# Performance work log

Hardware: AMD Instinct MI355X
Metric: run time of the kernel (lower is better)

The kernel has to match this reference:

```python
import jax, jax.numpy as jnp
import numpy as np

B, N = 4096, 8192
PULSE_LO = 40.0 / 60.0   # Hz
PULSE_HI = 250.0 / 60.0  # Hz


def setup_inputs() -> dict:
    key = jax.random.key(0)
    k1, k2 = jax.random.split(key)
    outputs = jax.random.normal(k1, (B, N), dtype=jnp.float32)
    # reference heart rates in Hz, uniform inside the pulse band
    targets = jax.random.uniform(k2, (B, 1), dtype=jnp.float32,
                                 minval=PULSE_LO, maxval=PULSE_HI)
    return {"outputs": outputs, "targets": targets, "Fs": 20}


def reference(outputs, targets, Fs):
    n = outputs.shape[-1]
    F = n // 2 + 1
    f = jnp.linspace(0.0, Fs / 2.0, F, dtype=jnp.float32)  # [F]

    min_idx = jnp.argmin(jnp.abs(f - PULSE_LO))
    max_idx = jnp.argmin(jnp.abs(f - PULSE_HI))

    # normalized rFFT power spectrum (torch.rfft(..., normalized=True) divides by sqrt(N))
    X = jnp.fft.rfft(outputs) * (1.0 / np.sqrt(n))          # [B, F] complex
    P1 = X.real ** 2 + X.imag ** 2                          # [B, F]

    # per-sample reference bin index
    r = jnp.argmin(jnp.abs(f[None, :] - targets.reshape(-1, 1)), axis=1)  # [B]
    rb = r[:, None]                                         # [B, 1]
    i = jnp.arange(F)[None, :]                              # [1, F]

    # signal mask u: 1 at ref and 1st harmonic, 0.5 at ref+-1 (applied after, as in torch)
    u = jnp.where((i == rb - 1) | (i == rb + 1), 0.5,
                  jnp.where((i == rb) | (i == 2 * rb), 1.0, 0.0))
    # noise mask w = 1 - u, zeroed outside pulse band and around 1st harmonic
    w = jnp.where((i < min_idx) | (i >= max_idx) |
                  (i == 2 * rb - 1) | (i == 2 * rb + 1),
                  0.0, 1.0 - u)

    signal_energy = jnp.sum(P1 * u, axis=1)                 # [B]
    noise_energy = jnp.sum(P1 * w, axis=1)                  # [B]
    losses = -10.0 * jnp.log(signal_energy / (noise_energy + 1.0)) / jnp.log(10.0)
    return jnp.mean(losses)
```

## Files before the change

### kernel.cpp

```cpp
#include <hip/hip_runtime.h>
#include <math.h>

#define TPB 256

typedef float cplx __attribute__((ext_vector_type(2)));

__device__ __forceinline__ cplx cmul(cplx a, cplx b) {
    return a.xx * b + cplx{-a.y, a.y} * b.yx;
}

__device__ __forceinline__ int sw2(int i) { return i ^ ((i >> 4) & 15); }

__device__ __forceinline__ void dft4(cplx& a, cplx& b, cplx& c, cplx& d) {
    cplx t0 = a + c, t1 = a - c, t2 = b + d, t3 = b - d;
    a = t0 + t2;
    c = t0 - t2;
    cplx jt3 = cplx{t3.y, -t3.x};
    b = t1 + jt3;
    d = t1 - jt3;
}

__device__ __forceinline__ void dft16(cplx v[16]) {
#pragma unroll
    for (int j = 0; j < 4; ++j) dft4(v[j], v[4 + j], v[8 + j], v[12 + j]);
    const float C1 = 0.9238795325112867f, S1 = 0.3826834323650898f;
    const float R2 = 0.7071067811865476f;
    v[5]  = cmul(v[5],  cplx{ C1, -S1});
    v[9]  = cmul(v[9],  cplx{ R2, -R2});
    v[13] = cmul(v[13], cplx{ S1, -C1});
    v[6]  = cmul(v[6],  cplx{ R2, -R2});
    v[10] = cplx{v[10].y, -v[10].x};
    v[14] = cmul(v[14], cplx{-R2, -R2});
    v[7]  = cmul(v[7],  cplx{ S1, -C1});
    v[11] = cmul(v[11], cplx{-R2, -R2});
    v[15] = cmul(v[15], cplx{-C1,  S1});
#pragma unroll
    for (int b = 0; b < 4; ++b) dft4(v[4 * b], v[4 * b + 1], v[4 * b + 2], v[4 * b + 3]);
}

__global__ __launch_bounds__(TPB, 4) void snr_kernel(const float* __restrict__ x,
                                                     const float* __restrict__ targets,
                                                     float* __restrict__ out) {
    __shared__ __align__(16) cplx Z[4096];
    float* zf = (float*)Z;

    const int t = threadIdx.x;
    const int blk = blockIdx.x;

    int r;
    {
        float tg = targets[blk];
        const float df = 0.00244140625f;
        int c0 = (int)(tg * 409.6f) - 2;
        if (c0 < 0) c0 = 0;
        r = c0;
        float best = fabsf(df * (float)c0 - tg);
        for (int i = c0 + 1; i <= c0 + 4 && i <= 4096; ++i) {
            float dd = fabsf(df * (float)i - tg);
            if (dd < best) { best = dd; r = i; }
        }
    }

    cplx v[16];
    const cplx* row = (const cplx*)(x + (size_t)blk * 8192);
#pragma unroll
    for (int l = 0; l < 16; ++l) v[l] = row[t + 256 * l];

    dft16(v);
    {
        float ang = -1.5339807878856412e-3f * (float)t;
        float sn, cs; __sincosf(ang, &sn, &cs);
        cplx w1 = cplx{cs, sn};
        cplx w2 = cmul(w1, w1), w3 = cmul(w2, w1);
        cplx w4 = cmul(w2, w2), w8 = cmul(w4, w4), w12 = cmul(w8, w4);
        cplx wa[4] = {cplx{1.f, 0.f}, w1, w2, w3};
        cplx wb[4] = {cplx{1.f, 0.f}, w4, w8, w12};
#pragma unroll
        for (int m = 0; m < 16; ++m) {
            Z[sw2(16 * t + m)] = cmul(v[4 * (m & 3) + (m >> 2)], cmul(wb[m >> 2], wa[m & 3]));
        }
    }
    __syncthreads();

#pragma unroll
    for (int l = 0; l < 16; ++l) v[l] = Z[sw2(t + 256 * l)];
    __syncthreads();
    dft16(v);
    {
        const int p = t >> 4, q = t & 15;
        float ang = -0.02454369260617026f * (float)p;
        float sn, cs; __sincosf(ang, &sn, &cs);
        cplx w1 = cplx{cs, sn};
        cplx w2 = cmul(w1, w1), w3 = cmul(w2, w1);
        cplx w4 = cmul(w2, w2), w8 = cmul(w4, w4), w12 = cmul(w8, w4);
        cplx wa[4] = {cplx{1.f, 0.f}, w1, w2, w3};
        cplx wb[4] = {cplx{1.f, 0.f}, w4, w8, w12};
#pragma unroll
        for (int m = 0; m < 16; ++m) {
            Z[sw2(q + 256 * p + 16 * m)] = cmul(v[4 * (m & 3) + (m >> 2)], cmul(wb[m >> 2], wa[m & 3]));
        }
    }
    __syncthreads();

#pragma unroll
    for (int l = 0; l < 16; ++l) v[l] = Z[sw2(t + 256 * l)];
    __syncthreads();
    dft16(v);
#pragma unroll
    for (int m = 0; m < 16; ++m) {
        Z[sw2(t + 256 * m)] = v[4 * (m & 3) + (m >> 2)];
    }
    __syncthreads();

    const int r2 = 2 * r;
    float band = 0.f;
    float p1cap = 0.f, p2cap = 0.f;
    int d1cap = -1, d2cap = -1;
    {
        float ang = -7.669903939428206e-4f * (float)t;
        float sn, cs; __sincosf(ang, &sn, &cs);
        cplx wk = cplx{cs, sn};
        const cplx wstep = cplx{0.9807852804032304f, -0.19509032201612825f};
#pragma unroll
        for (int m = 0; m < 16; ++m) {
            int k = t + 256 * m;
            cplx Zk = v[4 * (m & 3) + (m >> 2)];
            cplx Zn = Z[sw2((4096 - k) & 4095)];
            cplx Znc = cplx{Zn.x, -Zn.y};
            cplx s  = Zk + Znc;
            cplx dd = Zk - Znc;
            cplx tt = cmul(wk, dd);
            cplx X  = 0.5f * (s + cplx{tt.y, -tt.x});
            float P = (X.x * X.x + X.y * X.y) * (1.0f / 8192.0f);
            if ((unsigned)(k - 273) <= 1433u) band += P;
            int d1 = k - (r - 1);
            if ((unsigned)d1 < 3u) { d1cap = d1; p1cap = P; }
            int d2 = k - (r2 - 1);
            if ((unsigned)d2 < 3u) { d2cap = d2; p2cap = P; }
            wk = cmul(wk, wstep);
        }
    }
    __syncthreads();

    if (d1cap >= 0) zf[d1cap] = p1cap;
    if (d2cap >= 0) zf[3 + d2cap] = p2cap;

#pragma unroll
    for (int off = 32; off > 0; off >>= 1) band += __shfl_down(band, off);
    if ((t & 63) == 0) zf[8 + (t >> 6)] = band;
    __syncthreads();

    if (t == 0) {
        float bb = zf[8] + zf[9] + zf[10] + zf[11];
        float S = zf[1] + zf[4] + 0.5f * (zf[0] + zf[2]);
        float noise = bb;
        if (r <= 1706)      noise -= zf[1];
        if (r - 1 >= 273)   noise -= 0.5f * zf[0];
        if (r + 1 <= 1706)  noise -= 0.5f * zf[2];
        if (r2 - 1 <= 1706) noise -= zf[3];
        if (r2 <= 1706)     noise -= zf[4];
        if (r2 + 1 <= 1706) noise -= zf[5];
        float loss = -10.0f * log10f(S / (noise + 1.0f));
        atomicAdd(out, loss * (1.0f / 4096.0f));
    }
}

extern "C" void kernel_launch(void* const* d_in, const int* in_sizes, int n_in,
                              void* d_out, int out_size, void* d_ws, size_t ws_size,
                              hipStream_t stream) {
    const float* x = (const float*)d_in[0];
    const float* tg = (const float*)d_in[1];
    float* out = (float*)d_out;
    hipMemsetAsync(out, 0, sizeof(float), stream);
    snr_kernel<<<4096, TPB, 0, stream>>>(x, tg, out);
}
```

Measured before the change: 212.8 us.

## Halve shared memory by two-phase transposes and pair bins in postprocessing

Cuts the FFT scratch buffer from 4096 to 2048 complex entries. Each transpose is now done in two halves, with the low and high thread groups taking turns and extra barriers between them. The goal is to free LDS so more blocks fit on each CU. The final real-FFT step also changes: threads 0..128 each compute both bin k and its mirror 4096-k, so the remaining threads do no work there. This adds more __syncthreads calls, a second register array and branch divergence. The shared buffer aliasing and the sign choice for the mirrored bin are subtle and could hide correctness errors.

```diff
diff --git a/kernel.cpp b/kernel.cpp
--- a/kernel.cpp
+++ b/kernel.cpp
@@ -19,6 +19,8 @@
     b = t1 + jt3;
     d = t1 - jt3;
 }
+
+#define T16(j) (4 * ((j) & 3) + ((j) >> 2))
 
 __device__ __forceinline__ void dft16(cplx v[16]) {
 #pragma unroll
@@ -41,11 +43,13 @@
 __global__ __launch_bounds__(TPB, 4) void snr_kernel(const float* __restrict__ x,
                                                      const float* __restrict__ targets,
                                                      float* __restrict__ out) {
-    __shared__ __align__(16) cplx Z[4096];
+    __shared__ __align__(16) cplx Z[2048];
     float* zf = (float*)Z;
 
     const int t = threadIdx.x;
     const int blk = blockIdx.x;
+    const int u7 = t & 127;
+    const bool lo = (t < 128);
 
     int r;
     {
@@ -61,12 +65,12 @@
         }
     }
 
-    cplx v[16];
+    cplx a[16], b[16];
     const cplx* row = (const cplx*)(x + (size_t)blk * 8192);
 #pragma unroll
-    for (int l = 0; l < 16; ++l) v[l] = row[t + 256 * l];
-
-    dft16(v);
+    for (int l = 0; l < 16; ++l) a[l] = row[t + 256 * l];
+
+    dft16(a);
     {
         float ang = -1.5339807878856412e-3f * (float)t;
         float sn, cs; __sincosf(ang, &sn, &cs);
@@ -76,18 +80,31 @@
         cplx wa[4] = {cplx{1.f, 0.f}, w1, w2, w3};
         cplx wb[4] = {cplx{1.f, 0.f}, w4, w8, w12};
 #pragma unroll
-        for (int m = 0; m < 16; ++m) {
-            Z[sw2(16 * t + m)] = cmul(v[4 * (m & 3) + (m >> 2)], cmul(wb[m >> 2], wa[m & 3]));
-        }
-    }
-    __syncthreads();
-
-#pragma unroll
-    for (int l = 0; l < 16; ++l) v[l] = Z[sw2(t + 256 * l)];
-    __syncthreads();
-    dft16(v);
-    {
-        const int p = t >> 4, q = t & 15;
+        for (int m = 1; m < 16; ++m) {
+            int j = T16(m);
+            a[j] = cmul(a[j], cmul(wb[m >> 2], wa[m & 3]));
+        }
+    }
+    if (lo) {
+#pragma unroll
+        for (int j = 0; j < 16; ++j) Z[sw2(16 * u7 + T16(j))] = a[j];
+    }
+    __syncthreads();
+#pragma unroll
+    for (int l = 0; l < 8; ++l) b[l] = Z[sw2(t + 256 * l)];
+    __syncthreads();
+    if (!lo) {
+#pragma unroll
+        for (int j = 0; j < 16; ++j) Z[sw2(16 * u7 + T16(j))] = a[j];
+    }
+    __syncthreads();
+#pragma unroll
+    for (int l = 8; l < 16; ++l) b[l] = Z[sw2(t + 256 * (l - 8))];
+    __syncthreads();
+
+    dft16(b);
+    {
+        const int p = t >> 4;
         float ang = -0.02454369260617026f * (float)p;
         float sn, cs; __sincosf(ang, &sn, &cs);
         cplx w1 = cplx{cs, sn};
@@ -96,54 +113,83 @@
         cplx wa[4] = {cplx{1.f, 0.f}, w1, w2, w3};
         cplx wb[4] = {cplx{1.f, 0.f}, w4, w8, w12};
 #pragma unroll
-        for (int m = 0; m < 16; ++m) {
-            Z[sw2(q + 256 * p + 16 * m)] = cmul(v[4 * (m & 3) + (m >> 2)], cmul(wb[m >> 2], wa[m & 3]));
-        }
-    }
-    __syncthreads();
-
-#pragma unroll
-    for (int l = 0; l < 16; ++l) v[l] = Z[sw2(t + 256 * l)];
-    __syncthreads();
-    dft16(v);
-#pragma unroll
-    for (int m = 0; m < 16; ++m) {
-        Z[sw2(t + 256 * m)] = v[4 * (m & 3) + (m >> 2)];
+        for (int m = 1; m < 16; ++m) {
+            int j = T16(m);
+            b[j] = cmul(b[j], cmul(wb[m >> 2], wa[m & 3]));
+        }
+    }
+    {
+        const int ebase = (t & 15) + ((t & 0x70) << 4);
+        if (lo) {
+#pragma unroll
+            for (int j = 0; j < 16; ++j) Z[sw2(ebase + 16 * T16(j))] = b[j];
+        }
+        __syncthreads();
+#pragma unroll
+        for (int l = 0; l < 8; ++l) a[l] = Z[sw2(t + 256 * l)];
+        __syncthreads();
+        if (!lo) {
+#pragma unroll
+            for (int j = 0; j < 16; ++j) Z[sw2(ebase + 16 * T16(j))] = b[j];
+        }
+        __syncthreads();
+#pragma unroll
+        for (int l = 8; l < 16; ++l) a[l] = Z[sw2(t + 256 * (l - 8))];
+        __syncthreads();
+    }
+
+    dft16(a);
+
+    if (t > 128) {
+#pragma unroll
+        for (int j = 0; j < 16; ++j) Z[sw2(16 * u7 + T16(j))] = a[j];
     }
     __syncthreads();
 
     const int r2 = 2 * r;
     float band = 0.f;
-    float p1cap = 0.f, p2cap = 0.f;
-    int d1cap = -1, d2cap = -1;
-    {
+    float p1c = 0.f, p2c = 0.f, p1cn = 0.f, p2cn = 0.f;
+    int d1c = -1, d2c = -1, d1cn = -1, d2cn = -1;
+    if (t <= 128) {
+        const int mEnd = (t == 0) ? 9 : ((t == 128) ? 8 : 16);
+        const int pb = 16 * ((128 - t) & 127);
         float ang = -7.669903939428206e-4f * (float)t;
         float sn, cs; __sincosf(ang, &sn, &cs);
         cplx wk = cplx{cs, sn};
         const cplx wstep = cplx{0.9807852804032304f, -0.19509032201612825f};
 #pragma unroll
         for (int m = 0; m < 16; ++m) {
-            int k = t + 256 * m;
-            cplx Zk = v[4 * (m & 3) + (m >> 2)];
-            cplx Zn = Z[sw2((4096 - k) & 4095)];
-            cplx Znc = cplx{Zn.x, -Zn.y};
-            cplx s  = Zk + Znc;
-            cplx dd = Zk - Znc;
-            cplx tt = cmul(wk, dd);
-            cplx X  = 0.5f * (s + cplx{tt.y, -tt.x});
-            float P = (X.x * X.x + X.y * X.y) * (1.0f / 8192.0f);
-            if ((unsigned)(k - 273) <= 1433u) band += P;
-            int d1 = k - (r - 1);
-            if ((unsigned)d1 < 3u) { d1cap = d1; p1cap = P; }
-            int d2 = k - (r2 - 1);
-            if ((unsigned)d2 < 3u) { d2cap = d2; p2cap = P; }
+            if (m < mEnd) {
+                const int k = t + 256 * m;
+                const int nk = 4096 - k;
+                cplx Zk = a[T16(m)];
+                cplx Zn;
+                if (t == 0)        Zn = a[T16((16 - m) & 15)];
+                else if (t == 128) Zn = a[T16(15 - m)];
+                else               Zn = Z[sw2(pb + (15 - m))];
+                cplx Znc = cplx{Zn.x, -Zn.y};
+                cplx s  = Zk + Znc;
+                cplx dd = Zk - Znc;
+                cplx tt = cmul(wk, dd);
+                cplx Xk = s + cplx{ tt.y, -tt.x};
+                cplx Xn = s + cplx{-tt.y,  tt.x};
+                float Pk = (Xk.x * Xk.x + Xk.y * Xk.y) * (1.0f / 32768.0f);
+                float Pn = (Xn.x * Xn.x + Xn.y * Xn.y) * (1.0f / 32768.0f);
+                if ((unsigned)(k  - 273) <= 1433u) band += Pk;
+                if ((unsigned)(nk - 273) <= 1433u) band += Pn;
+                int d1 = k  - (r - 1);  if ((unsigned)d1 < 3u) { d1c  = d1; p1c  = Pk; }
+                int d2 = k  - (r2 - 1); if ((unsigned)d2 < 3u) { d2c  = d2; p2c  = Pk; }
+                int e1 = nk - (r - 1);  if ((unsigned)e1 < 3u) { d1cn = e1; p1cn = Pn; }
+                int e2 = nk - (r2 - 1); if ((unsigned)e2 < 3u) { d2cn = e2; p2cn = Pn; }
+            }
             wk = cmul(wk, wstep);
         }
     }
-    __syncthreads();
-
-    if (d1cap >= 0) zf[d1cap] = p1cap;
-    if (d2cap >= 0) zf[3 + d2cap] = p2cap;
+
+    if (d1c  >= 0) zf[d1c]      = p1c;
+    if (d2c  >= 0) zf[3 + d2c]  = p2c;
+    if (d1cn >= 0) zf[d1cn]     = p1cn;
+    if (d2cn >= 0) zf[3 + d2cn] = p2cn;
 
 #pragma unroll
     for (int off = 32; off > 0; off >>= 1) band += __shfl_down(band, off);
```

Result: slower. 218.3 us (+2.6%).

## Restrict spectrum post-processing to pulse band and compute harmonic bins separately

Applied to the files above, without the earlier changes.

The final post-processing loop now covers only the six m-slices that overlap the pulse band instead of all sixteen. Each twiddle comes from a constant table rather than a running complex multiply. The six reference and harmonic bins are computed directly by six dedicated threads instead of being captured inside the loop. The swizzle is changed to XOR only the low nibble within 16-element rows, and the twiddle multiply for index 0 is skipped. This reduces post-FFT arithmetic and LDS reads, with some risk of error in the new index and symmetry handling for harmonic bins above 2048.

```diff
diff --git a/kernel.cpp b/kernel.cpp
--- a/kernel.cpp
+++ b/kernel.cpp
@@ -8,8 +8,6 @@
 __device__ __forceinline__ cplx cmul(cplx a, cplx b) {
     return a.xx * b + cplx{-a.y, a.y} * b.yx;
 }
-
-__device__ __forceinline__ int sw2(int i) { return i ^ ((i >> 4) & 15); }
 
 __device__ __forceinline__ void dft4(cplx& a, cplx& b, cplx& c, cplx& d) {
     cplx t0 = a + c, t1 = a - c, t2 = b + d, t3 = b - d;
@@ -19,6 +17,8 @@
     b = t1 + jt3;
     d = t1 - jt3;
 }
+
+#define T16(j) (4 * ((j) & 3) + ((j) >> 2))
 
 __device__ __forceinline__ void dft16(cplx v[16]) {
 #pragma unroll
@@ -46,6 +46,7 @@
 
     const int t = threadIdx.x;
     const int blk = blockIdx.x;
+    const int tl = t & 15;
 
     int r;
     {
@@ -61,12 +62,12 @@
         }
     }
 
-    cplx v[16];
+    cplx a[16];
     const cplx* row = (const cplx*)(x + (size_t)blk * 8192);
 #pragma unroll
-    for (int l = 0; l < 16; ++l) v[l] = row[t + 256 * l];
-
-    dft16(v);
+    for (int l = 0; l < 16; ++l) a[l] = row[t + 256 * l];
+
+    dft16(a);
     {
         float ang = -1.5339807878856412e-3f * (float)t;
         float sn, cs; __sincosf(ang, &sn, &cs);
@@ -76,18 +77,25 @@
         cplx wa[4] = {cplx{1.f, 0.f}, w1, w2, w3};
         cplx wb[4] = {cplx{1.f, 0.f}, w4, w8, w12};
 #pragma unroll
-        for (int m = 0; m < 16; ++m) {
-            Z[sw2(16 * t + m)] = cmul(v[4 * (m & 3) + (m >> 2)], cmul(wb[m >> 2], wa[m & 3]));
-        }
-    }
-    __syncthreads();
-
-#pragma unroll
-    for (int l = 0; l < 16; ++l) v[l] = Z[sw2(t + 256 * l)];
-    __syncthreads();
-    dft16(v);
-    {
-        const int p = t >> 4, q = t & 15;
+        for (int m = 1; m < 16; ++m) {
+            int j = T16(m);
+            a[j] = cmul(a[j], cmul(wb[m >> 2], wa[m & 3]));
+        }
+    }
+    {
+        const int wb0 = t << 4;
+#pragma unroll
+        for (int j = 0; j < 16; ++j) Z[wb0 + (T16(j) ^ tl)] = a[j];
+    }
+    __syncthreads();
+
+    const int rb = t ^ ((t >> 4) & 15);
+#pragma unroll
+    for (int l = 0; l < 16; ++l) a[l] = Z[rb + (l << 8)];
+    __syncthreads();
+    dft16(a);
+    {
+        const int p = t >> 4;
         float ang = -0.02454369260617026f * (float)p;
         float sn, cs; __sincosf(ang, &sn, &cs);
         cplx w1 = cplx{cs, sn};
@@ -96,54 +104,84 @@
         cplx wa[4] = {cplx{1.f, 0.f}, w1, w2, w3};
         cplx wb[4] = {cplx{1.f, 0.f}, w4, w8, w12};
 #pragma unroll
+        for (int m = 1; m < 16; ++m) {
+            int j = T16(m);
+            a[j] = cmul(a[j], cmul(wb[m >> 2], wa[m & 3]));
+        }
+    }
+    {
+        const int base1 = (t >> 4) << 8;
+#pragma unroll
         for (int m = 0; m < 16; ++m) {
-            Z[sw2(q + 256 * p + 16 * m)] = cmul(v[4 * (m & 3) + (m >> 2)], cmul(wb[m >> 2], wa[m & 3]));
-        }
-    }
-    __syncthreads();
-
-#pragma unroll
-    for (int l = 0; l < 16; ++l) v[l] = Z[sw2(t + 256 * l)];
-    __syncthreads();
-    dft16(v);
-#pragma unroll
-    for (int m = 0; m < 16; ++m) {
-        Z[sw2(t + 256 * m)] = v[4 * (m & 3) + (m >> 2)];
-    }
-    __syncthreads();
-
-    const int r2 = 2 * r;
+            Z[base1 + (m << 4) + (tl ^ m)] = a[T16(m)];
+        }
+    }
+    __syncthreads();
+
+#pragma unroll
+    for (int l = 0; l < 16; ++l) a[l] = Z[rb + (l << 8)];
+    __syncthreads();
+    dft16(a);
+
+    {
+        const int wb0 = t << 4;
+#pragma unroll
+        for (int j = 0; j < 16; ++j) Z[wb0 + (T16(j) ^ tl)] = a[j];
+    }
+    __syncthreads();
+
     float band = 0.f;
-    float p1cap = 0.f, p2cap = 0.f;
-    int d1cap = -1, d2cap = -1;
     {
         float ang = -7.669903939428206e-4f * (float)t;
         float sn, cs; __sincosf(ang, &sn, &cs);
-        cplx wk = cplx{cs, sn};
-        const cplx wstep = cplx{0.9807852804032304f, -0.19509032201612825f};
-#pragma unroll
-        for (int m = 0; m < 16; ++m) {
-            int k = t + 256 * m;
-            cplx Zk = v[4 * (m & 3) + (m >> 2)];
-            cplx Zn = Z[sw2((4096 - k) & 4095)];
+        cplx wku = cplx{cs, sn};
+        const float WCc[7] = {1.f, 0.9807852804032304f, 0.9238795325112867f,
+                              0.8314696123025452f, 0.7071067811865476f,
+                              0.5555702330196022f, 0.3826834323650898f};
+        const float WCs[7] = {0.f, -0.19509032201612825f, -0.3826834323650898f,
+                              -0.5555702330196022f, -0.7071067811865476f,
+                              -0.8314696123025452f, -0.9238795325112867f};
+        const int pc = ((256 - t) & 255) << 4;
+        const int pl = (16 - tl) & 15;
+#pragma unroll
+        for (int m = 1; m <= 6; ++m) {
+            const int k = t + (m << 8);
+            const int za = t ? (pc | ((15 - m) ^ pl)) : (16 - m);
+            cplx Zk = a[T16(m)];
+            cplx Zn = Z[za];
+            cplx wk = cmul(wku, cplx{WCc[m], WCs[m]});
             cplx Znc = cplx{Zn.x, -Zn.y};
             cplx s  = Zk + Znc;
             cplx dd = Zk - Znc;
             cplx tt = cmul(wk, dd);
-            cplx X  = 0.5f * (s + cplx{tt.y, -tt.x});
-            float P = (X.x * X.x + X.y * X.y) * (1.0f / 8192.0f);
+            cplx X  = s + cplx{tt.y, -tt.x};
+            float P = (X.x * X.x + X.y * X.y) * (1.0f / 32768.0f);
             if ((unsigned)(k - 273) <= 1433u) band += P;
-            int d1 = k - (r - 1);
-            if ((unsigned)d1 < 3u) { d1cap = d1; p1cap = P; }
-            int d2 = k - (r2 - 1);
-            if ((unsigned)d2 < 3u) { d2cap = d2; p2cap = P; }
-            wk = cmul(wk, wstep);
-        }
-    }
-    __syncthreads();
-
-    if (d1cap >= 0) zf[d1cap] = p1cap;
-    if (d2cap >= 0) zf[3 + d2cap] = p2cap;
+        }
+    }
+
+    float capP = 0.f;
+    if (t < 6) {
+        const int c = (t < 3) ? (r - 1 + t) : (2 * r - 4 + t);
+        const int kk = (c <= 2048) ? c : (4096 - c);
+        const int nb = (4096 - kk) & 4095;
+        const int zka = ((kk & 255) << 4) | ((kk >> 8) ^ (kk & 15));
+        const int zna = ((nb & 255) << 4) | ((nb >> 8) ^ (nb & 15));
+        cplx Zk = Z[zka], Zn = Z[zna];
+        float ang = -7.669903939428206e-4f * (float)kk;
+        float sn, cs; __sincosf(ang, &sn, &cs);
+        cplx wk = cplx{cs, sn};
+        cplx Znc = cplx{Zn.x, -Zn.y};
+        cplx s  = Zk + Znc;
+        cplx dd = Zk - Znc;
+        cplx tt = cmul(wk, dd);
+        cplx X  = (c <= 2048) ? (s + cplx{tt.y, -tt.x})
+                              : (s + cplx{-tt.y, tt.x});
+        capP = (X.x * X.x + X.y * X.y) * (1.0f / 32768.0f);
+    }
+    __syncthreads();
+
+    if (t < 6) zf[t] = capP;
 
 #pragma unroll
     for (int off = 32; off > 0; off >>= 1) band += __shfl_down(band, off);
@@ -154,6 +192,7 @@
         float bb = zf[8] + zf[9] + zf[10] + zf[11];
         float S = zf[1] + zf[4] + 0.5f * (zf[0] + zf[2]);
         float noise = bb;
+        const int r2 = 2 * r;
         if (r <= 1706)      noise -= zf[1];
         if (r - 1 >= 273)   noise -= 0.5f * zf[0];
         if (r + 1 <= 1706)  noise -= 0.5f * zf[2];
```

Result: no change. 209.2 us (-1.7%).

## Compute each row's FFT in a single wavefront with 64-point register radix

Applied to the files above, without the earlier changes.

Each row's 4096-point complex FFT now runs in one 64-thread wavefront. It uses two register-resident radix-64 passes with one shared-memory transpose, which replaces the three radix-16 passes and the block-wide barriers. The real-to-complex post-processing uses lane shuffles to fetch mirrored bins, and it skips bins outside the pulse band unless they hold needed harmonic captures. The final mean goes through 64 spread-out atomic slots plus a last-block reduction instead of one contended atomic. In exchange, each thread holds 64 complex values in registers, which risks spills or low occupancy, and the code relies on wavefront-synchronous LDS behaviour in place of __syncthreads.

```diff
diff --git a/kernel.cpp b/kernel.cpp
--- a/kernel.cpp
+++ b/kernel.cpp
@@ -1,15 +1,13 @@
 #include <hip/hip_runtime.h>
 #include <math.h>
 
-#define TPB 256
+#define TPB 64
 
 typedef float cplx __attribute__((ext_vector_type(2)));
 
 __device__ __forceinline__ cplx cmul(cplx a, cplx b) {
     return a.xx * b + cplx{-a.y, a.y} * b.yx;
 }
-
-__device__ __forceinline__ int sw2(int i) { return i ^ ((i >> 4) & 15); }
 
 __device__ __forceinline__ void dft4(cplx& a, cplx& b, cplx& c, cplx& d) {
     cplx t0 = a + c, t1 = a - c, t2 = b + d, t3 = b - d;
@@ -20,7 +18,10 @@
     d = t1 - jt3;
 }
 
-__device__ __forceinline__ void dft16(cplx v[16]) {
+#define T16(j) (4 * ((j) & 3) + ((j) >> 2))
+#define R64(k) (16 * ((k) & 3) + T16((k) >> 2))
+
+__device__ __forceinline__ void dft16(cplx* v) {
 #pragma unroll
     for (int j = 0; j < 4; ++j) dft4(v[j], v[4 + j], v[8 + j], v[12 + j]);
     const float C1 = 0.9238795325112867f, S1 = 0.3826834323650898f;
@@ -38,18 +39,79 @@
     for (int b = 0; b < 4; ++b) dft4(v[4 * b], v[4 * b + 1], v[4 * b + 2], v[4 * b + 3]);
 }
 
-__global__ __launch_bounds__(TPB, 4) void snr_kernel(const float* __restrict__ x,
+__device__ constexpr float W64C[48] = {
+    1.f, 0.9951847267f, 0.9807852804f, 0.9569403357f, 0.9238795325f, 0.8819212643f,
+    0.8314696123f, 0.7730104534f, 0.7071067812f, 0.6343932842f, 0.5555702330f,
+    0.4713967368f, 0.3826834324f, 0.2902846773f, 0.1950903220f, 0.0980171403f,
+    0.f, -0.0980171403f, -0.1950903220f, -0.2902846773f, -0.3826834324f,
+    -0.4713967368f, -0.5555702330f, -0.6343932842f, -0.7071067812f, -0.7730104534f,
+    -0.8314696123f, -0.8819212643f, -0.9238795325f, -0.9569403357f, -0.9807852804f,
+    -0.9951847267f, -1.f, -0.9951847267f, -0.9807852804f, -0.9569403357f,
+    -0.9238795325f, -0.8819212643f, -0.8314696123f, -0.7730104534f, -0.7071067812f,
+    -0.6343932842f, -0.5555702330f, -0.4713967368f, -0.3826834324f, -0.2902846773f,
+    -0.1950903220f, -0.0980171403f};
+__device__ constexpr float W64S[48] = {
+    0.f, 0.0980171403f, 0.1950903220f, 0.2902846773f, 0.3826834324f, 0.4713967368f,
+    0.5555702330f, 0.6343932842f, 0.7071067812f, 0.7730104534f, 0.8314696123f,
+    0.8819212643f, 0.9238795325f, 0.9569403357f, 0.9807852804f, 0.9951847267f,
+    1.f, 0.9951847267f, 0.9807852804f, 0.9569403357f, 0.9238795325f, 0.8819212643f,
+    0.8314696123f, 0.7730104534f, 0.7071067812f, 0.6343932842f, 0.5555702330f,
+    0.4713967368f, 0.3826834324f, 0.2902846773f, 0.1950903220f, 0.0980171403f,
+    0.f, -0.0980171403f, -0.1950903220f, -0.2902846773f, -0.3826834324f,
+    -0.4713967368f, -0.5555702330f, -0.6343932842f, -0.7071067812f, -0.7730104534f,
+    -0.8314696123f, -0.8819212643f, -0.9238795325f, -0.9569403357f, -0.9807852804f,
+    -0.9951847267f};
+
+__device__ constexpr float W128C[33] = {
+    1.f, 0.9987954562f, 0.9951847267f, 0.9891765100f, 0.9807852804f, 0.9700312532f,
+    0.9569403357f, 0.9415440652f, 0.9238795325f, 0.9039892931f, 0.8819212643f,
+    0.8577286100f, 0.8314696123f, 0.8032075315f, 0.7730104534f, 0.7409511254f,
+    0.7071067812f, 0.6715589548f, 0.6343932842f, 0.5956993045f, 0.5555702330f,
+    0.5141027442f, 0.4713967368f, 0.4275550934f, 0.3826834324f, 0.3368898534f,
+    0.2902846773f, 0.2429801799f, 0.1950903220f, 0.1467304745f, 0.0980171403f,
+    0.0490676743f, 0.f};
+__device__ constexpr float W128S[33] = {
+    0.f, 0.0490676743f, 0.0980171403f, 0.1467304745f, 0.1950903220f, 0.2429801799f,
+    0.2902846773f, 0.3368898534f, 0.3826834324f, 0.4275550934f, 0.4713967368f,
+    0.5141027442f, 0.5555702330f, 0.5956993045f, 0.6343932842f, 0.6715589548f,
+    0.7071067812f, 0.7409511254f, 0.7730104534f, 0.8032075315f, 0.8314696123f,
+    0.8577286100f, 0.8819212643f, 0.9039892931f, 0.9238795325f, 0.9415440652f,
+    0.9569403357f, 0.9700312532f, 0.9807852804f, 0.9891765100f, 0.9951847267f,
+    0.9987954562f, 1.f};
+
+__device__ __forceinline__ void dft64(cplx v[64]) {
+#pragma unroll
+    for (int j = 0; j < 16; ++j) dft4(v[j], v[j + 16], v[j + 32], v[j + 48]);
+#pragma unroll
+    for (int s = 1; s < 4; ++s) {
+#pragma unroll
+        for (int j = 1; j < 16; ++j) {
+            const int n = j * s;
+            v[j + 16 * s] = cmul(v[j + 16 * s], cplx{W64C[n], -W64S[n]});
+        }
+    }
+#pragma unroll
+    for (int s = 0; s < 4; ++s) dft16(v + 16 * s);
+}
+
+__global__ __launch_bounds__(TPB, 2) void snr_kernel(const float* __restrict__ x,
                                                      const float* __restrict__ targets,
-                                                     float* __restrict__ out) {
-    __shared__ __align__(16) cplx Z[4096];
-    float* zf = (float*)Z;
-
-    const int t = threadIdx.x;
-    const int blk = blockIdx.x;
+                                                     float* __restrict__ out,
+                                                     float* __restrict__ ws) {
+    __shared__ __align__(16) cplx W[4096];
+    float* zf = (float*)W;
+
+    const int l = threadIdx.x;
+    const int bid = blockIdx.x;
+
+    cplx v[64];
+    const cplx* row = (const cplx*)(x + (size_t)bid * 8192);
+#pragma unroll
+    for (int j = 0; j < 64; ++j) v[j] = row[l + (j << 6)];
 
     int r;
     {
-        float tg = targets[blk];
+        float tg = targets[bid];
         const float df = 0.00244140625f;
         int c0 = (int)(tg * 409.6f) - 2;
         if (c0 < 0) c0 = 0;
@@ -60,100 +122,93 @@
             if (dd < best) { best = dd; r = i; }
         }
     }
-
-    cplx v[16];
-    const cplx* row = (const cplx*)(x + (size_t)blk * 8192);
-#pragma unroll
-    for (int l = 0; l < 16; ++l) v[l] = row[t + 256 * l];
-
-    dft16(v);
-    {
-        float ang = -1.5339807878856412e-3f * (float)t;
-        float sn, cs; __sincosf(ang, &sn, &cs);
+    const int r2 = 2 * r;
+
+    unsigned long long pm = 0;
+    {
+        int capb[6] = {r - 1, r, r + 1, r2 - 1, r2, r2 + 1};
+#pragma unroll
+        for (int i = 0; i < 6; ++i) {
+            int c = capb[i];
+            int kk = (c <= 2048) ? c : 4096 - c;
+            pm |= 1ull << (kk >> 6);
+        }
+    }
+
+    dft64(v);
+
+    cplx wA[8], wB[8];
+    {
+        float sn, cs;
+        __sincosf(-1.5339807878856412e-3f * (float)l, &sn, &cs);
         cplx w1 = cplx{cs, sn};
-        cplx w2 = cmul(w1, w1), w3 = cmul(w2, w1);
-        cplx w4 = cmul(w2, w2), w8 = cmul(w4, w4), w12 = cmul(w8, w4);
-        cplx wa[4] = {cplx{1.f, 0.f}, w1, w2, w3};
-        cplx wb[4] = {cplx{1.f, 0.f}, w4, w8, w12};
-#pragma unroll
-        for (int m = 0; m < 16; ++m) {
-            Z[sw2(16 * t + m)] = cmul(v[4 * (m & 3) + (m >> 2)], cmul(wb[m >> 2], wa[m & 3]));
-        }
-    }
-    __syncthreads();
-
-#pragma unroll
-    for (int l = 0; l < 16; ++l) v[l] = Z[sw2(t + 256 * l)];
-    __syncthreads();
-    dft16(v);
-    {
-        const int p = t >> 4, q = t & 15;
-        float ang = -0.02454369260617026f * (float)p;
-        float sn, cs; __sincosf(ang, &sn, &cs);
-        cplx w1 = cplx{cs, sn};
-        cplx w2 = cmul(w1, w1), w3 = cmul(w2, w1);
-        cplx w4 = cmul(w2, w2), w8 = cmul(w4, w4), w12 = cmul(w8, w4);
-        cplx wa[4] = {cplx{1.f, 0.f}, w1, w2, w3};
-        cplx wb[4] = {cplx{1.f, 0.f}, w4, w8, w12};
-#pragma unroll
-        for (int m = 0; m < 16; ++m) {
-            Z[sw2(q + 256 * p + 16 * m)] = cmul(v[4 * (m & 3) + (m >> 2)], cmul(wb[m >> 2], wa[m & 3]));
-        }
-    }
-    __syncthreads();
-
-#pragma unroll
-    for (int l = 0; l < 16; ++l) v[l] = Z[sw2(t + 256 * l)];
-    __syncthreads();
-    dft16(v);
-#pragma unroll
-    for (int m = 0; m < 16; ++m) {
-        Z[sw2(t + 256 * m)] = v[4 * (m & 3) + (m >> 2)];
-    }
-    __syncthreads();
-
-    const int r2 = 2 * r;
+        wA[0] = cplx{1.f, 0.f};
+#pragma unroll
+        for (int b = 1; b < 8; ++b) wA[b] = cmul(wA[b - 1], w1);
+        cplx w8 = cmul(wA[7], w1);
+        wB[0] = cplx{1.f, 0.f};
+#pragma unroll
+        for (int a = 1; a < 8; ++a) wB[a] = cmul(wB[a - 1], w8);
+    }
+
+#pragma unroll
+    for (int q = 0; q < 64; ++q) {
+        cplx val = v[R64(q)];
+        if (q != 0) {
+            cplx tw = (q < 8) ? wA[q]
+                      : (((q & 7) == 0) ? wB[q >> 3] : cmul(wB[q >> 3], wA[q & 7]));
+            val = cmul(val, tw);
+        }
+        W[((l + q) & 63) + (q << 6)] = val;
+    }
+    asm volatile("s_waitcnt lgkmcnt(0)" ::: "memory");
+#pragma unroll
+    for (int j = 0; j < 64; ++j) v[j] = W[((j + l) & 63) + (l << 6)];
+
+    dft64(v);
+
     float band = 0.f;
-    float p1cap = 0.f, p2cap = 0.f;
-    int d1cap = -1, d2cap = -1;
-    {
-        float ang = -7.669903939428206e-4f * (float)t;
-        float sn, cs; __sincosf(ang, &sn, &cs);
-        cplx wk = cplx{cs, sn};
-        const cplx wstep = cplx{0.9807852804032304f, -0.19509032201612825f};
-#pragma unroll
-        for (int m = 0; m < 16; ++m) {
-            int k = t + 256 * m;
-            cplx Zk = v[4 * (m & 3) + (m >> 2)];
-            cplx Zn = Z[sw2((4096 - k) & 4095)];
-            cplx Znc = cplx{Zn.x, -Zn.y};
-            cplx s  = Zk + Znc;
-            cplx dd = Zk - Znc;
-            cplx tt = cmul(wk, dd);
-            cplx X  = 0.5f * (s + cplx{tt.y, -tt.x});
-            float P = (X.x * X.x + X.y * X.y) * (1.0f / 8192.0f);
-            if ((unsigned)(k - 273) <= 1433u) band += P;
-            int d1 = k - (r - 1);
-            if ((unsigned)d1 < 3u) { d1cap = d1; p1cap = P; }
-            int d2 = k - (r2 - 1);
-            if ((unsigned)d2 < 3u) { d2cap = d2; p2cap = P; }
-            wk = cmul(wk, wstep);
-        }
-    }
-    __syncthreads();
-
-    if (d1cap >= 0) zf[d1cap] = p1cap;
-    if (d2cap >= 0) zf[3 + d2cap] = p2cap;
+    cplx wl;
+    {
+        float sn, cs;
+        __sincosf(-7.669903939428206e-4f * (float)l, &sn, &cs);
+        wl = cplx{cs, sn};
+    }
+    const int plane = (64 - l) & 63;
+#pragma unroll
+    for (int p = 4; p <= 32; ++p) {
+        if (p > 26 && !((pm >> p) & 1)) continue;
+        cplx Zk = v[R64(p)];
+        cplx Zn;
+        Zn.x = __shfl(v[R64(63 - p)].x, plane);
+        Zn.y = __shfl(v[R64(63 - p)].y, plane);
+        if (l == 0) Zn = v[R64((64 - p) & 63)];
+        cplx wk = cmul(wl, cplx{W128C[p], -W128S[p]});
+        cplx Znc = cplx{Zn.x, -Zn.y};
+        cplx s  = Zk + Znc;
+        cplx dd = Zk - Znc;
+        cplx tt = cmul(wk, dd);
+        cplx Xk = s + cplx{tt.y, -tt.x};
+        float Pk = (Xk.x * Xk.x + Xk.y * Xk.y) * (1.0f / 32768.0f);
+        if (p >= 5 && p <= 25) band += Pk;
+        else if (p == 4)  { if (l >= 17) band += Pk; }
+        else if (p == 26) { if (l <= 42) band += Pk; }
+        const int k = l + (p << 6);
+        int d1 = k - (r - 1);  if ((unsigned)d1 < 3u) zf[d1] = Pk;
+        int d2 = k - (r2 - 1); if ((unsigned)d2 < 3u) zf[3 + d2] = Pk;
+        cplx Xn = s + cplx{-tt.y, tt.x};
+        float Pn = (Xn.x * Xn.x + Xn.y * Xn.y) * (1.0f / 32768.0f);
+        int e2 = (4096 - k) - (r2 - 1); if ((unsigned)e2 < 3u) zf[3 + e2] = Pn;
+    }
 
 #pragma unroll
     for (int off = 32; off > 0; off >>= 1) band += __shfl_down(band, off);
-    if ((t & 63) == 0) zf[8 + (t >> 6)] = band;
-    __syncthreads();
-
-    if (t == 0) {
-        float bb = zf[8] + zf[9] + zf[10] + zf[11];
+
+    asm volatile("s_waitcnt lgkmcnt(0)" ::: "memory");
+    unsigned c = 0;
+    if (l == 0) {
         float S = zf[1] + zf[4] + 0.5f * (zf[0] + zf[2]);
-        float noise = bb;
+        float noise = band;
         if (r <= 1706)      noise -= zf[1];
         if (r - 1 >= 273)   noise -= 0.5f * zf[0];
         if (r + 1 <= 1706)  noise -= 0.5f * zf[2];
@@ -161,7 +216,17 @@
         if (r2 <= 1706)     noise -= zf[4];
         if (r2 + 1 <= 1706) noise -= zf[5];
         float loss = -10.0f * log10f(S / (noise + 1.0f));
-        atomicAdd(out, loss * (1.0f / 4096.0f));
+        atomicAdd(&ws[bid & 63], loss * (1.0f / 4096.0f));
+        __threadfence();
+        c = atomicAdd((unsigned*)(ws + 64), 1u) + 1;
+    }
+    c = __shfl(c, 0);
+    if (c == (unsigned)gridDim.x) {
+        __threadfence();
+        float sv = ws[l];
+#pragma unroll
+        for (int off = 32; off > 0; off >>= 1) sv += __shfl_down(sv, off);
+        if (l == 0) out[0] = sv;
     }
 }
 
@@ -171,6 +236,7 @@
     const float* x = (const float*)d_in[0];
     const float* tg = (const float*)d_in[1];
     float* out = (float*)d_out;
-    hipMemsetAsync(out, 0, sizeof(float), stream);
-    snr_kernel<<<4096, TPB, 0, stream>>>(x, tg, out);
-}
+    float* ws = (float*)d_ws;
+    hipMemsetAsync(ws, 0, 65 * sizeof(float), stream);
+    snr_kernel<<<4096, TPB, 0, stream>>>(x, tg, out, ws);
+}
```

Result: slower. 349.6 us (+64.3%).
